# Kernel optimization log

Measured on AMD Instinct MI355X. Metric: run time of the kernel, lower is better.

The kernel has to match this reference:

```python
import jax, jax.numpy as jnp
import numpy as np


def setup_inputs() -> dict:
    key = jax.random.key(0)
    ks = jax.random.split(key, 5)
    B, M, R = 32, 32, 128
    d_lang, d_region, d_rank, d_fusion = 1024, 2048, 256, 256
    u = jax.random.normal(ks[0], (B, M, d_lang), dtype=jnp.float32)
    v = jax.random.normal(ks[1], (B, R, d_region), dtype=jnp.float32)
    # Linear weights stored torch-style as (out_features, in_features)
    Wu = jax.random.normal(ks[2], (d_rank, d_lang), dtype=jnp.float32) * (1.0 / np.sqrt(d_lang))
    Wv = jax.random.normal(ks[3], (d_rank, d_region), dtype=jnp.float32) * (1.0 / np.sqrt(d_region))
    Wp = jax.random.normal(ks[4], (d_fusion, d_rank), dtype=jnp.float32) * (1.0 / np.sqrt(d_rank))
    bp = jnp.zeros((d_fusion,), dtype=jnp.float32)
    return {"u": u, "v": v, "Wu": Wu, "Wv": Wv, "Wp": Wp, "bp": bp}


def reference(u, v, Wu, Wv, Wp, bp):
    # u: (B, M, d_lang), v: (B, R, d_region)
    up = jnp.einsum('bmd,rd->bmr', u, Wu)          # (B, M, d_rank)  [rd: out x in]
    vp = jnp.einsum('bnd,rd->bnr', v, Wv)          # (B, R, d_rank)
    # broadcast bilinear multiply: (B, M, R, d_rank)
    prod = up[:, :, None, :] * vp[:, None, :, :]
    o = jnp.einsum('bmnk,fk->bmnf', prod, Wp) + bp  # p-linear -> (B, M, R, d_fusion)
    # dropout is identity in inference mode
    return jax.nn.relu(o)
```

## Files before the change

kernel.cpp:

```cpp
#include <hip/hip_runtime.h>
#include <hip/hip_bf16.h>


typedef __attribute__((ext_vector_type(8))) short short8;
typedef __attribute__((ext_vector_type(4))) float floatx4;
typedef __attribute__((ext_vector_type(4))) unsigned uintx4;

__device__ __forceinline__ short f2bf(float f) {
    union { float f; unsigned u; } cv; cv.f = f;
    unsigned r = cv.u + 0x7fffu + ((cv.u >> 16) & 1u);
    return (short)(r >> 16);
}
__device__ __forceinline__ float bf2f(short s) {
    union { unsigned u; float f; } cv;
    cv.u = ((unsigned)(unsigned short)s) << 16; return cv.f;
}
__device__ __forceinline__ unsigned trunc2(float a, float b) {
    return __builtin_amdgcn_perm(__float_as_uint(b), __float_as_uint(a), 0x07060302);
}
__device__ __forceinline__ unsigned rne2(float a, float b) {
    unsigned ua = __float_as_uint(a); ua += 0x7fffu + ((ua >> 16) & 1u);
    unsigned ub = __float_as_uint(b); ub += 0x7fffu + ((ub >> 16) & 1u);
    return __builtin_amdgcn_perm(ub, ua, 0x07060302);
}

#define GL2LDS(gptr, lptr) __builtin_amdgcn_global_load_lds(                    \
    (const __attribute__((address_space(1))) void*)(gptr),                      \
    (__attribute__((address_space(3))) void*)(lptr), 16, 0, 0)

#define N_U  1048576
#define N_V  8388608
#define N_WU 262144
#define N_WV 524288

__global__ __launch_bounds__(256) void convert_kernel(
    const float* __restrict__ u, const float* __restrict__ v,
    const float* __restrict__ Wu, const float* __restrict__ Wv,
    short* __restrict__ dst)
{
    const int n_u = N_U / 4, n_v = N_V / 4, n_wu = N_WU / 4, n_wv = N_WV / 4;
    const int total = n_u + n_v + n_wu + n_wv;
    for (int i4 = blockIdx.x * blockDim.x + threadIdx.x; i4 < total;
         i4 += gridDim.x * blockDim.x) {
        const float* src; int off = i4;
        if (off < n_u) src = u;
        else { off -= n_u;
            if (off < n_v) src = v;
            else { off -= n_v;
                if (off < n_wu) src = Wu;
                else { off -= n_wu; src = Wv; } } }
        float4 f = *((const float4*)src + off);
        uint2 o;
        o.x = rne2(f.x, f.y);
        o.y = rne2(f.z, f.w);
        *((uint2*)dst + i4) = o;
    }
}

__global__ __launch_bounds__(256) void proj_kernel(
    const short* __restrict__ Xu, const short* __restrict__ Wgu,
    short* __restrict__ Cu,
    const short* __restrict__ Xv, const short* __restrict__ Wgv,
    short* __restrict__ Cv)
{
    __shared__ short Xs[64 * 32];
    __shared__ short Wsh[64 * 32];

    const int tid  = threadIdx.x;
    const int lane = tid & 63;
    const int wave = tid >> 6;
    const int quad = lane >> 4;
    const int l15  = lane & 15;

    int blk = blockIdx.x;
    const short *X, *W; short* C; int D;
    if (blk < 64) { X = Xu; W = Wgu; C = Cu; D = 1024; }
    else          { blk -= 64; X = Xv; W = Wgv; C = Cv; D = 2048; }
    const int r0 = (blk >> 2) * 64;
    const int c0 = (blk & 3) * 64;
    const int wr = (wave >> 1) * 32;
    const int wc = (wave & 1) * 32;

    const int sr  = tid >> 2;
    const int skg = (tid & 3) * 8;

    floatx4 acc[2][2] = {};

    for (int kc = 0; kc < D; kc += 32) {
        __syncthreads();
        GL2LDS(X + (size_t)(r0 + sr) * D + kc + skg, &Xs[sr * 32 + skg]);
        GL2LDS(W + (size_t)(c0 + sr) * D + kc + skg, &Wsh[sr * 32 + skg]);
        __syncthreads();

        short8 a[2], bfr[2];
#pragma unroll
        for (int t = 0; t < 2; t++)
            a[t] = *(const short8*)&Xs[(wr + t * 16 + l15) * 32 + quad * 8];
#pragma unroll
        for (int t = 0; t < 2; t++)
            bfr[t] = *(const short8*)&Wsh[(wc + t * 16 + l15) * 32 + quad * 8];
#pragma unroll
        for (int tn = 0; tn < 2; tn++)
#pragma unroll
            for (int tf = 0; tf < 2; tf++)
                acc[tn][tf] = __builtin_amdgcn_mfma_f32_16x16x32_bf16(
                    bfr[tf], a[tn], acc[tn][tf], 0, 0, 0);
    }

#pragma unroll
    for (int tn = 0; tn < 2; tn++)
#pragma unroll
        for (int tf = 0; tf < 2; tf++) {
            int xrow  = r0 + wr + tn * 16 + l15;
            int cbase = c0 + wc + tf * 16 + quad * 4;
            uint2 pk;
            pk.x = rne2(acc[tn][tf][0], acc[tn][tf][1]);
            pk.y = rne2(acc[tn][tf][2], acc[tn][tf][3]);
            *(uint2*)&C[(size_t)xrow * 256 + cbase] = pk;
        }
}

__global__ __launch_bounds__(256) void bilinear_kernel(
    const short* __restrict__ up, const short* __restrict__ vp,
    const float* __restrict__ Wp, const float* __restrict__ bp,
    float* __restrict__ out)
{
    __shared__ short vp_s[2][128 * 32];
    __shared__ short Ws[128 * 72];
    __shared__ float up_s[256];

    const int tid  = threadIdx.x;
    const int lane = tid & 63;
    const int wave = tid >> 6;
    const int quad = lane >> 4;
    const int l15  = lane & 15;

    const int f_blk = blockIdx.x & 1;
    const int bm    = blockIdx.x >> 1;
    const int b     = bm >> 5;
    const int f0    = f_blk * 128;
    const int wn    = (wave >> 1) * 64;
    const int wf    = (wave & 1) * 64;

    up_s[tid] = bf2f(up[(size_t)bm * 256 + tid]);

    const int sr   = tid >> 2;
    const int skg  = (tid & 3) * 8;
    const int wrow = tid >> 1;
    const int kh   = (tid & 1) * 32;

    floatx4 acc[4][4] = {};

    for (int kc = 0; kc < 256; kc += 64) {
        __syncthreads();
        {
            const short* g = vp + (size_t)(b * 128 + sr) * 256 + kc + skg;
            GL2LDS(g,                 &vp_s[0][sr * 32 + skg]);
            GL2LDS(g + 64 * 256,      &vp_s[0][(64 + sr) * 32 + skg]);
            GL2LDS(g + 32,            &vp_s[1][sr * 32 + skg]);
            GL2LDS(g + 64 * 256 + 32, &vp_s[1][(64 + sr) * 32 + skg]);
        }
        {
            const float* wpr = Wp + (size_t)(f0 + wrow) * 256 + kc + kh;
            const float* usr = &up_s[kc + kh];
#pragma unroll
            for (int h = 0; h < 4; h++) {
                float w[8], uu[8];
                *(float4*)&w[0]  = *(const float4*)(wpr + 8 * h);
                *(float4*)&w[4]  = *(const float4*)(wpr + 8 * h + 4);
                *(float4*)&uu[0] = *(const float4*)(usr + 8 * h);
                *(float4*)&uu[4] = *(const float4*)(usr + 8 * h + 4);
                uintx4 o;
#pragma unroll
                for (int i = 0; i < 4; i++)
                    o[i] = trunc2(w[2 * i] * uu[2 * i], w[2 * i + 1] * uu[2 * i + 1]);
                *(uintx4*)&Ws[wrow * 72 + kh + 8 * h] = o;
            }
        }
        __syncthreads();

#pragma unroll
        for (int kk2 = 0; kk2 < 2; kk2++) {
            short8 a[4], bfr[4];
#pragma unroll
            for (int t = 0; t < 4; t++)
                a[t] = *(const short8*)&vp_s[kk2][(wn + t * 16 + l15) * 32 + quad * 8];
#pragma unroll
            for (int t = 0; t < 4; t++)
                bfr[t] = *(const short8*)&Ws[(wf + t * 16 + l15) * 72 + kk2 * 32 + quad * 8];
#pragma unroll
            for (int tn = 0; tn < 4; tn++)
#pragma unroll
                for (int tf = 0; tf < 4; tf++)
                    acc[tn][tf] = __builtin_amdgcn_mfma_f32_16x16x32_bf16(
                        bfr[tf], a[tn], acc[tn][tf], 0, 0, 0);
        }
    }

    float4 bpv[4];
#pragma unroll
    for (int tf = 0; tf < 4; tf++)
        bpv[tf] = *(const float4*)&bp[f0 + wf + tf * 16 + quad * 4];

    const size_t out_base = (size_t)bm * 128 * 256;
#pragma unroll
    for (int tn = 0; tn < 4; tn++) {
        const int n = wn + tn * 16 + l15;
        float* orow = out + out_base + (size_t)n * 256;
#pragma unroll
        for (int tf = 0; tf < 4; tf++) {
            const int fbase = f0 + wf + tf * 16 + quad * 4;
            float4 o;
            o.x = fmaxf(acc[tn][tf][0] + bpv[tf].x, 0.0f);
            o.y = fmaxf(acc[tn][tf][1] + bpv[tf].y, 0.0f);
            o.z = fmaxf(acc[tn][tf][2] + bpv[tf].z, 0.0f);
            o.w = fmaxf(acc[tn][tf][3] + bpv[tf].w, 0.0f);
            *(float4*)(orow + fbase) = o;
        }
    }
}

extern "C" void kernel_launch(void* const* d_in, const int* in_sizes, int n_in,
                              void* d_out, int out_size, void* d_ws, size_t ws_size,
                              hipStream_t stream) {
    const float* u  = (const float*)d_in[0];
    const float* v  = (const float*)d_in[1];
    const float* Wu = (const float*)d_in[2];
    const float* Wv = (const float*)d_in[3];
    const float* Wp = (const float*)d_in[4];
    const float* bp = (const float*)d_in[5];
    float* out = (float*)d_out;

    short* bf    = (short*)d_ws;
    short* u_bf  = bf;
    short* v_bf  = u_bf + N_U;
    short* Wu_bf = v_bf + N_V;
    short* Wv_bf = Wu_bf + N_WU;
    short* up_bf = Wv_bf + N_WV;
    short* vp_bf = up_bf + 262144;

    convert_kernel<<<dim3(2048), dim3(256), 0, stream>>>(u, v, Wu, Wv, bf);
    proj_kernel<<<dim3(320), dim3(256), 0, stream>>>(
        u_bf, Wu_bf, up_bf, v_bf, Wv_bf, vp_bf);
    bilinear_kernel<<<dim3(2048), dim3(256), 0, stream>>>(
        up_bf, vp_bf, Wp, bp, out);
}
```

Baseline: 231.0 us.

## Batch proj K-slices per barrier and shrink bilinear LDS tiles to K=32

The projection GEMM now stages four 32-wide K slices per pair of barriers instead of one, so more global-to-LDS loads are in flight and there are fewer synchronisations. The bilinear kernel cuts its K step from 64 to 32, which roughly halves its LDS footprint and should let more blocks be resident per CU. It also issues the Wp global loads before the vp LDS copies so their latency can overlap. In exchange, the bilinear kernel needs twice as many barrier iterations, and the Ws row stride of 36 shorts makes its 16-byte LDS accesses not 16-byte aligned.

```diff
diff --git a/kernel.cpp b/kernel.cpp
--- a/kernel.cpp
+++ b/kernel.cpp
@@ -6,11 +6,6 @@
 typedef __attribute__((ext_vector_type(4))) float floatx4;
 typedef __attribute__((ext_vector_type(4))) unsigned uintx4;
 
-__device__ __forceinline__ short f2bf(float f) {
-    union { float f; unsigned u; } cv; cv.f = f;
-    unsigned r = cv.u + 0x7fffu + ((cv.u >> 16) & 1u);
-    return (short)(r >> 16);
-}
 __device__ __forceinline__ float bf2f(short s) {
     union { unsigned u; float f; } cv;
     cv.u = ((unsigned)(unsigned short)s) << 16; return cv.f;
@@ -63,8 +58,8 @@
     const short* __restrict__ Xv, const short* __restrict__ Wgv,
     short* __restrict__ Cv)
 {
-    __shared__ short Xs[64 * 32];
-    __shared__ short Wsh[64 * 32];
+    __shared__ short Xs[4][64 * 32];
+    __shared__ short Wsh[4][64 * 32];
 
     const int tid  = threadIdx.x;
     const int lane = tid & 63;
@@ -86,25 +81,33 @@
 
     floatx4 acc[2][2] = {};
 
-    for (int kc = 0; kc < D; kc += 32) {
-        __syncthreads();
-        GL2LDS(X + (size_t)(r0 + sr) * D + kc + skg, &Xs[sr * 32 + skg]);
-        GL2LDS(W + (size_t)(c0 + sr) * D + kc + skg, &Wsh[sr * 32 + skg]);
-        __syncthreads();
-
-        short8 a[2], bfr[2];
-#pragma unroll
-        for (int t = 0; t < 2; t++)
-            a[t] = *(const short8*)&Xs[(wr + t * 16 + l15) * 32 + quad * 8];
-#pragma unroll
-        for (int t = 0; t < 2; t++)
-            bfr[t] = *(const short8*)&Wsh[(wc + t * 16 + l15) * 32 + quad * 8];
-#pragma unroll
-        for (int tn = 0; tn < 2; tn++)
-#pragma unroll
-            for (int tf = 0; tf < 2; tf++)
-                acc[tn][tf] = __builtin_amdgcn_mfma_f32_16x16x32_bf16(
-                    bfr[tf], a[tn], acc[tn][tf], 0, 0, 0);
+    for (int kc = 0; kc < D; kc += 128) {
+        __syncthreads();
+        const size_t xoff = (size_t)(r0 + sr) * D + kc + skg;
+        const size_t woff = (size_t)(c0 + sr) * D + kc + skg;
+#pragma unroll
+        for (int s = 0; s < 4; s++) {
+            GL2LDS(X + xoff + s * 32, &Xs[s][sr * 32 + skg]);
+            GL2LDS(W + woff + s * 32, &Wsh[s][sr * 32 + skg]);
+        }
+        __syncthreads();
+
+#pragma unroll
+        for (int s = 0; s < 4; s++) {
+            short8 a[2], bfr[2];
+#pragma unroll
+            for (int t = 0; t < 2; t++)
+                a[t] = *(const short8*)&Xs[s][(wr + t * 16 + l15) * 32 + quad * 8];
+#pragma unroll
+            for (int t = 0; t < 2; t++)
+                bfr[t] = *(const short8*)&Wsh[s][(wc + t * 16 + l15) * 32 + quad * 8];
+#pragma unroll
+            for (int tn = 0; tn < 2; tn++)
+#pragma unroll
+                for (int tf = 0; tf < 2; tf++)
+                    acc[tn][tf] = __builtin_amdgcn_mfma_f32_16x16x32_bf16(
+                        bfr[tf], a[tn], acc[tn][tf], 0, 0, 0);
+        }
     }
 
 #pragma unroll
@@ -125,8 +128,8 @@
     const float* __restrict__ Wp, const float* __restrict__ bp,
     float* __restrict__ out)
 {
-    __shared__ short vp_s[2][128 * 32];
-    __shared__ short Ws[128 * 72];
+    __shared__ short vp_s[128 * 32];
+    __shared__ short Ws[128 * 36];
     __shared__ float up_s[256];
 
     const int tid  = threadIdx.x;
@@ -144,57 +147,58 @@
 
     up_s[tid] = bf2f(up[(size_t)bm * 256 + tid]);
 
-    const int sr   = tid >> 2;
-    const int skg  = (tid & 3) * 8;
-    const int wrow = tid >> 1;
-    const int kh   = (tid & 1) * 32;
+    const int sr  = tid >> 2;
+    const int skg = (tid & 3) * 8;
+    const int sn  = tid >> 1;
+    const int skh = (tid & 1) * 16;
 
     floatx4 acc[4][4] = {};
 
-    for (int kc = 0; kc < 256; kc += 64) {
-        __syncthreads();
+    for (int kc = 0; kc < 256; kc += 32) {
+        __syncthreads();
+        const float* wpr = Wp + (size_t)(f0 + sn) * 256 + kc + skh;
+        float w[16];
+        *(float4*)&w[0]  = *(const float4*)(wpr);
+        *(float4*)&w[4]  = *(const float4*)(wpr + 4);
+        *(float4*)&w[8]  = *(const float4*)(wpr + 8);
+        *(float4*)&w[12] = *(const float4*)(wpr + 12);
         {
             const short* g = vp + (size_t)(b * 128 + sr) * 256 + kc + skg;
-            GL2LDS(g,                 &vp_s[0][sr * 32 + skg]);
-            GL2LDS(g + 64 * 256,      &vp_s[0][(64 + sr) * 32 + skg]);
-            GL2LDS(g + 32,            &vp_s[1][sr * 32 + skg]);
-            GL2LDS(g + 64 * 256 + 32, &vp_s[1][(64 + sr) * 32 + skg]);
+            GL2LDS(g,            &vp_s[sr * 32 + skg]);
+            GL2LDS(g + 64 * 256, &vp_s[(64 + sr) * 32 + skg]);
         }
         {
-            const float* wpr = Wp + (size_t)(f0 + wrow) * 256 + kc + kh;
-            const float* usr = &up_s[kc + kh];
-#pragma unroll
-            for (int h = 0; h < 4; h++) {
-                float w[8], uu[8];
-                *(float4*)&w[0]  = *(const float4*)(wpr + 8 * h);
-                *(float4*)&w[4]  = *(const float4*)(wpr + 8 * h + 4);
-                *(float4*)&uu[0] = *(const float4*)(usr + 8 * h);
-                *(float4*)&uu[4] = *(const float4*)(usr + 8 * h + 4);
-                uintx4 o;
-#pragma unroll
-                for (int i = 0; i < 4; i++)
-                    o[i] = trunc2(w[2 * i] * uu[2 * i], w[2 * i + 1] * uu[2 * i + 1]);
-                *(uintx4*)&Ws[wrow * 72 + kh + 8 * h] = o;
-            }
-        }
-        __syncthreads();
-
-#pragma unroll
-        for (int kk2 = 0; kk2 < 2; kk2++) {
-            short8 a[4], bfr[4];
-#pragma unroll
-            for (int t = 0; t < 4; t++)
-                a[t] = *(const short8*)&vp_s[kk2][(wn + t * 16 + l15) * 32 + quad * 8];
-#pragma unroll
-            for (int t = 0; t < 4; t++)
-                bfr[t] = *(const short8*)&Ws[(wf + t * 16 + l15) * 72 + kk2 * 32 + quad * 8];
-#pragma unroll
-            for (int tn = 0; tn < 4; tn++)
-#pragma unroll
-                for (int tf = 0; tf < 4; tf++)
-                    acc[tn][tf] = __builtin_amdgcn_mfma_f32_16x16x32_bf16(
-                        bfr[tf], a[tn], acc[tn][tf], 0, 0, 0);
-        }
+            const float* usr = &up_s[kc + skh];
+            float uu[16];
+            *(float4*)&uu[0]  = *(const float4*)(usr);
+            *(float4*)&uu[4]  = *(const float4*)(usr + 4);
+            *(float4*)&uu[8]  = *(const float4*)(usr + 8);
+            *(float4*)&uu[12] = *(const float4*)(usr + 12);
+            uintx4 o0, o1;
+#pragma unroll
+            for (int i = 0; i < 4; i++)
+                o0[i] = trunc2(w[2 * i] * uu[2 * i], w[2 * i + 1] * uu[2 * i + 1]);
+#pragma unroll
+            for (int i = 0; i < 4; i++)
+                o1[i] = trunc2(w[8 + 2 * i] * uu[8 + 2 * i], w[9 + 2 * i] * uu[9 + 2 * i]);
+            *(uintx4*)&Ws[sn * 36 + skh]     = o0;
+            *(uintx4*)&Ws[sn * 36 + skh + 8] = o1;
+        }
+        __syncthreads();
+
+        short8 a[4], bfr[4];
+#pragma unroll
+        for (int t = 0; t < 4; t++)
+            a[t] = *(const short8*)&vp_s[(wn + t * 16 + l15) * 32 + quad * 8];
+#pragma unroll
+        for (int t = 0; t < 4; t++)
+            bfr[t] = *(const short8*)&Ws[(wf + t * 16 + l15) * 36 + quad * 8];
+#pragma unroll
+        for (int tn = 0; tn < 4; tn++)
+#pragma unroll
+            for (int tf = 0; tf < 4; tf++)
+                acc[tn][tf] = __builtin_amdgcn_mfma_f32_16x16x32_bf16(
+                    bfr[tf], a[tn], acc[tn][tf], 0, 0, 0);
     }
 
     float4 bpv[4];
```

After: 219.4 us. 5.0% less time.
